# Optimization experiments

Measured on AMD Instinct MI355X. Metric: run time of the kernel, lower is better.

Reference implementation:

```python
import jax, jax.numpy as jnp
import numpy as np

B, T, E, S, D, HG = 16, 1024, 1024, 256, 512, 128
P_MIN, P_MAX, K_MAX, MAX_INNOV, EPS = 1e-6, 10.0, 1.0, 10.0, 1e-6


def setup_inputs() -> dict:
    key = jax.random.key(0)
    ks = jax.random.split(key, 16)
    g = lambda k, shape, fan: jax.random.normal(k, shape, jnp.float32) * np.float32(1.0 / np.sqrt(fan))
    # orthogonal init for the state-transition matrix A
    A = jnp.linalg.qr(jax.random.normal(ks[1], (S, S), jnp.float32))[0]
    return {
        "x": jax.random.normal(ks[0], (B, T, E), jnp.float32),
        "W_in": g(ks[2], (E, D), E), "b_in": jnp.zeros((D,), jnp.float32),
        "W_state": g(ks[3], (D, S), D), "b_state": jnp.zeros((S,), jnp.float32),
        "A": A, "H": g(ks[4], (D, S), D),
        "Q": jnp.full((S,), 0.1, jnp.float32), "R": jnp.full((D,), 0.1, jnp.float32),
        "W_z": g(ks[5], (HG, HG + S), HG + S), "W_r": g(ks[6], (HG, HG + S), HG + S),
        "W_h": g(ks[7], (HG, HG + S), HG + S),
        "b_z": jnp.zeros((HG,), jnp.float32), "b_r": jnp.zeros((HG,), jnp.float32),
        "b_h": jnp.zeros((HG,), jnp.float32),
        "W_out": g(ks[8], (HG, S), HG),
        "W_outp": g(ks[9], (D, E), D), "b_outp": jnp.zeros((E,), jnp.float32),
    }


def reference(x, W_in, b_in, W_state, b_state, A, H, Q, R,
              W_z, W_r, W_h, b_z, b_r, b_h, W_out, W_outp, b_outp):
    # input projection with GELU (Dense(d_inner, activation='gelu'))
    u = jax.nn.gelu(jnp.einsum("bte,ed->btd", x, W_in) + b_in)  # [B,T,D]
    q_sp = jax.nn.softplus(Q)                 # process noise, per state dim
    r_eff = jnp.mean(jax.nn.softplus(R))      # scalar effective measurement noise

    def step(carry, u_t):
        x_est, P, h = carry                   # [B,S], [B,S], [B,HG]
        # 1. state prediction (+ learned control input from measurement)
        x_pred = x_est @ A.T + u_t @ W_state + b_state          # [B,S]
        # 2. covariance prediction with clipping
        P_pred = jnp.clip(P + q_sp, P_MIN, P_MAX)                # [B,S]
        # 3. innovation (clipped for stability)
        y = jnp.clip(u_t - x_pred @ H.T, -MAX_INNOV, MAX_INNOV)  # [B,D]
        # 4. Kalman gain, bounded in [0, k_max]
        K = jnp.clip(P_pred / (P_pred + r_eff + EPS), 0.0, K_MAX)  # [B,S]
        # 5. state update: x_post = x_pred + K * (H^T @ innovation)
        x_post = x_pred + K * (y @ H)                            # [B,S]
        # 6. covariance update
        P_post = jnp.clip(P_pred * (1.0 - K), P_MIN, P_MAX)      # [B,S]
        # GRU gating over posterior state
        hx = jnp.concatenate([h, x_post], axis=-1)               # [B,HG+S]
        zg = jax.nn.sigmoid(hx @ W_z.T + b_z)
        rg = jax.nn.sigmoid(hx @ W_r.T + b_r)
        hc = jnp.tanh(jnp.concatenate([rg * h, x_post], axis=-1) @ W_h.T + b_h)
        h_new = (1.0 - zg) * h + zg * hc                         # [B,HG]
        # neural correction of state via GRU output projection
        x_final = x_post + h_new @ W_out                         # [B,S]
        return (x_final, P_post, h_new), x_final

    x0 = jnp.zeros((x.shape[0], S), x.dtype)
    P0 = jnp.ones((x.shape[0], S), x.dtype)   # identity covariance (diagonal)
    h0 = jnp.zeros((x.shape[0], HG), x.dtype)
    (_, _, _), xs = jax.lax.scan(step, (x0, P0, h0), jnp.swapaxes(u, 0, 1))
    xs = jnp.swapaxes(xs, 0, 1)               # [B,T,S]
    obs = jnp.einsum("bts,ds->btd", xs, H)    # reconstruct observation space
    out = jnp.einsum("btd,de->bte", obs, W_outp) + b_outp
    return out + x                            # residual connection
```

## Files before the change

kernel.cpp:

```cpp
#include <hip/hip_runtime.h>
#include <cstdint>
#include <cstddef>

#define NB 16
#define NT 1024
#define NE 1024
#define NS 256
#define ND 512
#define NH 128
#define T0 16

#define OFF_US   ((size_t)0)
#define OFF_HU   ((size_t)4194304)
#define OFF_U3   ((size_t)8388608)
#define OFF_KT   ((size_t)12582912)
#define OFF_HT   ((size_t)12845056)
#define OFF_AT   ((size_t)12976128)
#define OFF_G    ((size_t)13041664)
#define OFF_IG   ((size_t)13107200)
#define OFF_MINF ((size_t)13172736)
#define OFF_WZT  ((size_t)13238272)
#define OFF_WRT  ((size_t)13287424)
#define OFF_WHT  ((size_t)13336576)
#define OFF_HTWO ((size_t)13385728)
#define OFF_PACK ((size_t)13647872)

#define PK_A   0
#define PK_G   65536
#define PK_M   131072
#define PK_Z   196608
#define PK_R   245760
#define PK_H   294912
#define PK_O   344064
#define PK_WIN 376832
#define PK_WST 901120
#define PK_HM  1032192
#define PK_HTW 1163264


typedef short bf16x8 __attribute__((ext_vector_type(8)));
typedef float f32x4 __attribute__((ext_vector_type(4)));
typedef unsigned int u32x2 __attribute__((ext_vector_type(2)));

#define MFMA(a, b, c) __builtin_amdgcn_mfma_f32_16x16x32_bf16((a), (b), (c), 0, 0, 0)

#define SYNCW() do { \
    __builtin_amdgcn_sched_barrier(0); \
    asm volatile("s_waitcnt lgkmcnt(0)" ::: "memory"); \
    __builtin_amdgcn_s_barrier(); \
    __builtin_amdgcn_sched_barrier(0); \
} while (0)

__device__ __forceinline__ float gelu_tanh(float v) {
    const float c = 0.7978845608028654f;
    float t = tanhf(c * (v + 0.044715f * v * v * v));
    return 0.5f * v * (1.0f + t);
}
__device__ __forceinline__ float softplus_f(float x) {
    if (x > 20.0f) return x;
    return log1pf(expf(x));
}
__device__ __forceinline__ short f2bf_s(float f) {
    unsigned u = __float_as_uint(f);
    u += 0x7fffu + ((u >> 16) & 1u);
    return (short)(u >> 16);
}
__device__ __forceinline__ unsigned pk_bf(float a, float b) {
    return ((unsigned)(unsigned short)f2bf_s(b) << 16) | (unsigned)(unsigned short)f2bf_s(a);
}
__device__ __forceinline__ float exp2_hw(float x) {
    float r; asm("v_exp_f32 %0, %1" : "=v"(r) : "v"(x)); return r;
}
__device__ __forceinline__ float rcp_hw(float x) {
    float r; asm("v_rcp_f32 %0, %1" : "=v"(r) : "v"(x)); return r;
}
__device__ __forceinline__ f32x4 sig4(f32x4 x) {
    f32x4 o;
#pragma unroll
    for (int i = 0; i < 4; ++i)
        o[i] = rcp_hw(1.0f + exp2_hw(-1.442695040888963f * x[i]));
    return o;
}
__device__ __forceinline__ f32x4 tanh4(f32x4 x) {
    f32x4 o;
#pragma unroll
    for (int i = 0; i < 4; ++i) {
        float e = exp2_hw(2.885390081777927f * x[i]);
        o[i] = 1.0f - 2.0f * rcp_hw(e + 1.0f);
    }
    return o;
}
__device__ __forceinline__ void st_bf4(char* base, int stride, int row, int byteoff,
                                       const f32x4& v) {
    u32x2 p;
    p[0] = pk_bf(v[0], v[1]);
    p[1] = pk_bf(v[2], v[3]);
    *(u32x2*)(base + row * stride + byteoff) = p;
}

#define BFRAG(buf, STR, ks) (*(const bf16x8*)((buf) + (l & 15) * (STR) + (ks) * 64 + (l >> 4) * 16))
#define GFRAG(p, fi) (*(const bf16x8*)((p) + ((size_t)(fi) * 64 + l) * 8))
#define LFRAG(buf, fi) (*(const bf16x8*)((buf) + (size_t)(fi) * 1024 + l * 16))

__global__ __launch_bounds__(512) void k_precompute(const float* __restrict__ Q,
                                                    const float* __restrict__ R,
                                                    float* __restrict__ Kt) {
    __shared__ float red[512];
    __shared__ float r_eff_sh;
    const int t = threadIdx.x;
    red[t] = softplus_f(R[t]);
    __syncthreads();
    for (int s = 256; s > 0; s >>= 1) {
        if (t < s) red[t] += red[t + s];
        __syncthreads();
    }
    if (t == 0) r_eff_sh = red[0] / 512.0f;
    __syncthreads();
    const float r_eff = r_eff_sh;
    if (t < NS) {
        const float q = softplus_f(Q[t]);
        float P = 1.0f;
        for (int step = 0; step < NT; ++step) {
            float Pp = fminf(fmaxf(P + q, 1e-6f), 10.0f);
            float K  = fminf(fmaxf(Pp / (Pp + r_eff + 1e-6f), 0.0f), 1.0f);
            Kt[(size_t)step * NS + t] = K;
            P = fminf(fmaxf(Pp * (1.0f - K), 1e-6f), 10.0f);
        }
    }
}

__global__ void k_transpose(const float* __restrict__ in, float* __restrict__ outp,
                            int Rr, int Cc) {
    int i = blockIdx.x * 256 + threadIdx.x;
    if (i < Rr * Cc) {
        int r = i / Cc, c = i % Cc;
        outp[(size_t)c * Rr + r] = in[i];
    }
}

__global__ void k_ig(const float* __restrict__ G, const float* __restrict__ Kt,
                     float* __restrict__ IG) {
    int i = blockIdx.x * 256 + threadIdx.x;
    if (i >= NS * NS) return;
    int r = i >> 8, c = i & 255;
    float kinf = Kt[(size_t)(NT - 1) * NS + c];
    IG[i] = ((r == c) ? 1.0f : 0.0f) - G[i] * kinf;
}

__global__ void k_fuse(const float* __restrict__ us, const float* __restrict__ usG,
                       const float* __restrict__ Hu, const float* __restrict__ Kt,
                       float* __restrict__ u3) {
    int i = blockIdx.x * 256 + threadIdx.x;
    if (i >= NT * NB * NS) return;
    int s = i & 255;
    int tm = i >> 8;
    int m = tm & 15, t = tm >> 4;
    size_t src = ((size_t)m * NT + t) * NS + s;
    float k = Kt[(size_t)t * NS + s];
    u3[i] = us[src] + k * (Hu[src] - usG[src]);
}

__global__ void k_pack(const float* __restrict__ W, short* __restrict__ dst, int K, int N) {
    int f = blockIdx.x * 256 + threadIdx.x;
    if (f >= K * N) return;
    const int j = f & 7, l = (f >> 3) & 63, tile = f >> 9;
    const int KS = K >> 5;
    const int nt = tile / KS, ks = tile - nt * KS;
    const int k = ks * 32 + (l >> 4) * 8 + j;
    const int n = nt * 16 + (l & 15);
    dst[f] = f2bf_s(W[(size_t)k * N + n]);
}

__global__ __launch_bounds__(256) void k_mm(const float* __restrict__ Af,
                                            const short* __restrict__ Bpk,
                                            const float* __restrict__ bias,
                                            const float* __restrict__ resid,
                                            float* __restrict__ C,
                                            int N, int K, int act) {
    const int tid = threadIdx.x, w = tid >> 6, l = tid & 63;
    const int KS = K >> 5;
    const int mt = blockIdx.x * 4 + w;
    const int nt0 = blockIdx.y * 8;
    const float* arow = Af + (size_t)(mt * 16 + (l & 15)) * K + ((l >> 4) * 8);
    f32x4 acc[8];
#pragma unroll
    for (int j = 0; j < 8; ++j) acc[j] = (f32x4){0.f, 0.f, 0.f, 0.f};
    for (int ks = 0; ks < KS; ++ks) {
        const float* ap = arow + ks * 32;
        f32x4 a0 = *(const f32x4*)ap;
        f32x4 a1 = *(const f32x4*)(ap + 4);
        union { bf16x8 v; unsigned u[4]; } au;
        au.u[0] = pk_bf(a0[0], a0[1]); au.u[1] = pk_bf(a0[2], a0[3]);
        au.u[2] = pk_bf(a1[0], a1[1]); au.u[3] = pk_bf(a1[2], a1[3]);
#pragma unroll
        for (int j = 0; j < 8; ++j) {
            bf16x8 b = *(const bf16x8*)(Bpk + ((size_t)(nt0 + j) * KS + ks) * 512 + (size_t)l * 8);
            acc[j] = MFMA(b, au.v, acc[j]);
        }
    }
    const int m = mt * 16 + (l & 15);
    const int lg = l >> 4;
#pragma unroll
    for (int j = 0; j < 8; ++j) {
        const int n = (nt0 + j) * 16 + lg * 4;
        f32x4 v = acc[j];
        if (bias) v += *(const f32x4*)(bias + n);
        if (act) {
#pragma unroll
            for (int r = 0; r < 4; ++r) v[r] = gelu_tanh(v[r]);
        }
        if (resid) v += *(const f32x4*)(resid + (size_t)m * N + n);
        *(f32x4*)(C + (size_t)m * N + n) = v;
    }
}

__global__ __launch_bounds__(256) void k_gemm(const float* __restrict__ Am,
                                              const float* __restrict__ Bm,
                                              const float* __restrict__ bias,
                                              const float* __restrict__ resid,
                                              float* __restrict__ Cm,
                                              int M, int N, int K, int act) {
    __shared__ __align__(16) float As[16][68];
    __shared__ __align__(16) float Bs[16][68];
    const int tid = threadIdx.x;
    const int bn = blockIdx.x, bm = blockIdx.y;
    const int row0 = bm * 64, col0 = bn * 64;
    const int tx = tid & 15, ty = tid >> 4;
    const int ar = tid >> 2, ac = (tid & 3) << 2;
    const int bk = tid >> 4, bc = (tid & 15) << 2;

    float acc[4][4];
#pragma unroll
    for (int i = 0; i < 4; ++i)
#pragma unroll
        for (int j = 0; j < 4; ++j) acc[i][j] = 0.0f;

    for (int k0 = 0; k0 < K; k0 += 16) {
        float4 av = *(const float4*)(Am + (size_t)(row0 + ar) * K + k0 + ac);
        float4 bv = *(const float4*)(Bm + (size_t)(k0 + bk) * N + col0 + bc);
        As[ac + 0][ar] = av.x; As[ac + 1][ar] = av.y;
        As[ac + 2][ar] = av.z; As[ac + 3][ar] = av.w;
        *(float4*)&Bs[bk][bc] = bv;
        __syncthreads();
#pragma unroll
        for (int kk = 0; kk < 16; ++kk) {
            const float a0 = As[kk][ty * 4 + 0], a1 = As[kk][ty * 4 + 1];
            const float a2 = As[kk][ty * 4 + 2], a3 = As[kk][ty * 4 + 3];
            const float4 b4 = *(const float4*)&Bs[kk][tx * 4];
            acc[0][0] += a0 * b4.x; acc[0][1] += a0 * b4.y; acc[0][2] += a0 * b4.z; acc[0][3] += a0 * b4.w;
            acc[1][0] += a1 * b4.x; acc[1][1] += a1 * b4.y; acc[1][2] += a1 * b4.z; acc[1][3] += a1 * b4.w;
            acc[2][0] += a2 * b4.x; acc[2][1] += a2 * b4.y; acc[2][2] += a2 * b4.z; acc[2][3] += a2 * b4.w;
            acc[3][0] += a3 * b4.x; acc[3][1] += a3 * b4.y; acc[3][2] += a3 * b4.z; acc[3][3] += a3 * b4.w;
        }
        __syncthreads();
    }
#pragma unroll
    for (int i = 0; i < 4; ++i) {
        const int r = row0 + ty * 4 + i;
#pragma unroll
        for (int j = 0; j < 4; ++j) {
            const int c = col0 + tx * 4 + j;
            float v = acc[i][j];
            if (bias) v += bias[c];
            if (act) v = gelu_tanh(v);
            if (resid) v += resid[(size_t)r * N + c];
            Cm[(size_t)r * N + c] = v;
        }
    }
}

#define XE_STR 528
#define HB_STR 272

__global__ __launch_bounds__(512, 2) void k_scan_mfma(
    const short* __restrict__ pM, const short* __restrict__ pA, const short* __restrict__ pG,
    const short* __restrict__ pZ, const short* __restrict__ pR, const short* __restrict__ pH,
    const short* __restrict__ pO,
    const float* __restrict__ bz, const float* __restrict__ br, const float* __restrict__ bh,
    const float* __restrict__ us, const float* __restrict__ Hu, const float* __restrict__ u3,
    const float* __restrict__ Kt, float* __restrict__ xs)
{
    __shared__ __align__(16) char XE[16 * XE_STR];
    __shared__ __align__(16) char XT[16 * XE_STR];
    __shared__ __align__(16) char HBs[16 * HB_STR];
    __shared__ __align__(16) char RGs[16 * HB_STR];
    __shared__ __align__(16) char WHH[64 * 1024];

    const int tid = threadIdx.x, w = tid >> 6, l = tid & 63;
    const int m = l & 15, lg = l >> 4;
    const int c0 = 32 * w + 4 * lg;
    const int cg = 16 * w + 4 * lg;

    for (int i = tid; i < (16 * XE_STR) / 4; i += 512) ((int*)XE)[i] = 0;
    for (int i = tid; i < (16 * HB_STR) / 4; i += 512) ((int*)HBs)[i] = 0;
    for (int i = tid; i < 4096; i += 512) {
        int fi = i >> 6, ln = i & 63;
        int wv = fi >> 3, ks = fi & 7;
        ((int4*)WHH)[i] = *(const int4*)(pH + ((size_t)(wv * 12 + 4 + ks) * 64 + ln) * 8);
    }

    const f32x4 bzv = *(const f32x4*)(bz + cg);
    const f32x4 brv = *(const f32x4*)(br + cg);
    const f32x4 bhv = *(const f32x4*)(bh + cg);
    f32x4 hFr = {0.f, 0.f, 0.f, 0.f};
    __syncthreads();

    for (int t = 0; t < T0; ++t) {
        const float* usb = us + ((size_t)m * NT + t) * NS;
        const float* hub = Hu + ((size_t)m * NT + t) * NS;
        const float* ktb = Kt + (size_t)t * NS;
        f32x4 us0 = *(const f32x4*)(usb + c0), us1 = *(const f32x4*)(usb + c0 + 16);
        f32x4 hu0 = *(const f32x4*)(hub + c0), hu1 = *(const f32x4*)(hub + c0 + 16);
        f32x4 kv0 = *(const f32x4*)(ktb + c0), kv1 = *(const f32x4*)(ktb + c0 + 16);
        f32x4 p0 = {0.f,0.f,0.f,0.f}, p1 = {0.f,0.f,0.f,0.f};
#pragma unroll
        for (int ks = 0; ks < 8; ++ks) {
            bf16x8 xe = BFRAG(XE, XE_STR, ks);
            p0 = MFMA(GFRAG(pA, (2 * w + 0) * 8 + ks), xe, p0);
            p1 = MFMA(GFRAG(pA, (2 * w + 1) * 8 + ks), xe, p1);
        }
        p0 += us0; p1 += us1;
        st_bf4(XT, XE_STR, m, c0 * 2, p0);
        st_bf4(XT, XE_STR, m, (c0 + 16) * 2, p1);
        SYNCW();
        f32x4 g0 = {0.f,0.f,0.f,0.f}, g1 = {0.f,0.f,0.f,0.f};
#pragma unroll
        for (int ks = 0; ks < 8; ++ks) {
            bf16x8 xt = BFRAG(XT, XE_STR, ks);
            g0 = MFMA(GFRAG(pG, (2 * w + 0) * 8 + ks), xt, g0);
            g1 = MFMA(GFRAG(pG, (2 * w + 1) * 8 + ks), xt, g1);
        }
        f32x4 xq0 = p0 + kv0 * (hu0 - g0);
        f32x4 xq1 = p1 + kv1 * (hu1 - g1);
        st_bf4(XE, XE_STR, m, c0 * 2, xq0);
        st_bf4(XE, XE_STR, m, (c0 + 16) * 2, xq1);
        SYNCW();
        f32x4 za = bzv, ra = brv, hx = bhv;
#pragma unroll
        for (int ks = 0; ks < 4; ++ks) {
            bf16x8 hb = BFRAG(HBs, HB_STR, ks);
            za = MFMA(GFRAG(pZ, w * 12 + ks), hb, za);
            ra = MFMA(GFRAG(pR, w * 12 + ks), hb, ra);
        }
#pragma unroll
        for (int ks = 0; ks < 8; ++ks) {
            bf16x8 xef = BFRAG(XE, XE_STR, ks);
            za = MFMA(GFRAG(pZ, w * 12 + 4 + ks), xef, za);
            ra = MFMA(GFRAG(pR, w * 12 + 4 + ks), xef, ra);
            hx = MFMA(GFRAG(pH, w * 12 + 4 + ks), xef, hx);
        }
        f32x4 z = sig4(za), r = sig4(ra), rg = r * hFr;
        st_bf4(RGs, HB_STR, m, cg * 2, rg);
        SYNCW();
        f32x4 hc = hx;
#pragma unroll
        for (int ks = 0; ks < 4; ++ks)
            hc = MFMA(GFRAG(pH, w * 12 + ks), BFRAG(RGs, HB_STR, ks), hc);
        f32x4 hcv = tanh4(hc);
        f32x4 hn = hFr + z * (hcv - hFr);
        hFr = hn;
        st_bf4(HBs, HB_STR, m, cg * 2, hn);
        SYNCW();
#pragma unroll
        for (int ks = 0; ks < 4; ++ks) {
            bf16x8 hb2 = BFRAG(HBs, HB_STR, ks);
            xq0 = MFMA(GFRAG(pO, (2 * w + 0) * 4 + ks), hb2, xq0);
            xq1 = MFMA(GFRAG(pO, (2 * w + 1) * 4 + ks), hb2, xq1);
        }
        st_bf4(XE, XE_STR, m, c0 * 2, xq0);
        st_bf4(XE, XE_STR, m, (c0 + 16) * 2, xq1);
        {
            float* xb = xs + ((size_t)m * NT + t) * NS;
            *(f32x4*)(xb + c0) = xq0;
            *(f32x4*)(xb + c0 + 16) = xq1;
        }
        SYNCW();
    }

    bf16x8 rM0[8], rM1[8], rZx[8], rRx[8], rZh[4], rRh[4], rO0[4], rO1[4], rHh[4];
#pragma unroll
    for (int ks = 0; ks < 8; ++ks) {
        rM0[ks] = GFRAG(pM, (2 * w + 0) * 8 + ks);
        rM1[ks] = GFRAG(pM, (2 * w + 1) * 8 + ks);
        rZx[ks] = GFRAG(pZ, w * 12 + 4 + ks);
        rRx[ks] = GFRAG(pR, w * 12 + 4 + ks);
    }
#pragma unroll
    for (int ks = 0; ks < 4; ++ks) {
        rZh[ks] = GFRAG(pZ, w * 12 + ks);
        rRh[ks] = GFRAG(pR, w * 12 + ks);
        rO0[ks] = GFRAG(pO, (2 * w + 0) * 4 + ks);
        rO1[ks] = GFRAG(pO, (2 * w + 1) * 4 + ks);
        rHh[ks] = GFRAG(pH, w * 12 + ks);
    }

    f32x4 zh = bzv, rh = brv;
#pragma unroll
    for (int ks = 0; ks < 4; ++ks) {
        bf16x8 hb = BFRAG(HBs, HB_STR, ks);
        zh = MFMA(rZh[ks], hb, zh);
        rh = MFMA(rRh[ks], hb, rh);
    }

    f32x4 cu0 = *(const f32x4*)(u3 + (size_t)T0 * (NB * NS) + (size_t)m * NS + c0);
    f32x4 cu1 = *(const f32x4*)(u3 + (size_t)T0 * (NB * NS) + (size_t)m * NS + c0 + 16);

    for (int t = T0; t < NT; ++t) {
        const int tn = (t + 1 < NT) ? (t + 1) : t;
        const float* ubn = u3 + (size_t)tn * (NB * NS) + (size_t)m * NS;
        f32x4 nx0 = *(const f32x4*)(ubn + c0);
        f32x4 nx1 = *(const f32x4*)(ubn + c0 + 16);

        f32x4 xq0 = {0.f,0.f,0.f,0.f}, xq1 = {0.f,0.f,0.f,0.f};
#pragma unroll
        for (int ks = 0; ks < 8; ++ks) {
            bf16x8 xe = BFRAG(XE, XE_STR, ks);
            xq0 = MFMA(rM0[ks], xe, xq0);
            xq1 = MFMA(rM1[ks], xe, xq1);
        }
        xq0 += cu0; xq1 += cu1;
        st_bf4(XT, XE_STR, m, c0 * 2, xq0);
        st_bf4(XT, XE_STR, m, (c0 + 16) * 2, xq1);
        SYNCW();
        f32x4 za = zh, ra = rh, hx = bhv;
#pragma unroll
        for (int ks = 0; ks < 8; ++ks) {
            bf16x8 xt = BFRAG(XT, XE_STR, ks);
            za = MFMA(rZx[ks], xt, za);
            ra = MFMA(rRx[ks], xt, ra);
            hx = MFMA(LFRAG(WHH, w * 8 + ks), xt, hx);
        }
        f32x4 z = sig4(za), r = sig4(ra), rg = r * hFr;
        st_bf4(RGs, HB_STR, m, cg * 2, rg);
        SYNCW();
        f32x4 hc = hx;
#pragma unroll
        for (int ks = 0; ks < 4; ++ks)
            hc = MFMA(rHh[ks], BFRAG(RGs, HB_STR, ks), hc);
        f32x4 hcv = tanh4(hc);
        f32x4 hn = hFr + z * (hcv - hFr);
        hFr = hn;
        st_bf4(HBs, HB_STR, m, cg * 2, hn);
        SYNCW();
        f32x4 zhN = bzv, rhN = brv;
#pragma unroll
        for (int ks = 0; ks < 4; ++ks) {
            bf16x8 hb2 = BFRAG(HBs, HB_STR, ks);
            xq0 = MFMA(rO0[ks], hb2, xq0);
            xq1 = MFMA(rO1[ks], hb2, xq1);
            zhN = MFMA(rZh[ks], hb2, zhN);
            rhN = MFMA(rRh[ks], hb2, rhN);
        }
        st_bf4(XE, XE_STR, m, c0 * 2, xq0);
        st_bf4(XE, XE_STR, m, (c0 + 16) * 2, xq1);
        {
            float* xb = xs + ((size_t)m * NT + t) * NS;
            *(f32x4*)(xb + c0) = xq0;
            *(f32x4*)(xb + c0 + 16) = xq1;
        }
        zh = zhN; rh = rhN;
        cu0 = nx0; cu1 = nx1;
        SYNCW();
    }
}

extern "C" void kernel_launch(void* const* d_in, const int* in_sizes, int n_in,
                              void* d_out, int out_size, void* d_ws, size_t ws_size,
                              hipStream_t stream) {
    (void)in_sizes; (void)n_in; (void)out_size; (void)ws_size;
    const float* x       = (const float*)d_in[0];
    const float* W_in    = (const float*)d_in[1];
    const float* b_in    = (const float*)d_in[2];
    const float* W_state = (const float*)d_in[3];
    const float* b_state = (const float*)d_in[4];
    const float* A       = (const float*)d_in[5];
    const float* H       = (const float*)d_in[6];
    const float* Q       = (const float*)d_in[7];
    const float* R       = (const float*)d_in[8];
    const float* W_z     = (const float*)d_in[9];
    const float* W_r     = (const float*)d_in[10];
    const float* W_h     = (const float*)d_in[11];
    const float* b_z     = (const float*)d_in[12];
    const float* b_r     = (const float*)d_in[13];
    const float* b_h     = (const float*)d_in[14];
    const float* W_out   = (const float*)d_in[15];
    const float* W_outp  = (const float*)d_in[16];
    const float* b_outp  = (const float*)d_in[17];
    float* out = (float*)d_out;
    float* w = (float*)d_ws;

    float* us   = w + OFF_US;
    float* Hu   = w + OFF_HU;
    float* u3   = w + OFF_U3;
    float* Kt   = w + OFF_KT;
    float* Ht   = w + OFF_HT;
    float* At   = w + OFF_AT;
    float* G    = w + OFF_G;
    float* IG   = w + OFF_IG;
    float* Minf = w + OFF_MINF;
    float* Wzt  = w + OFF_WZT;
    float* Wrt  = w + OFF_WRT;
    float* Wht  = w + OFF_WHT;
    float* HtWo = w + OFF_HTWO;
    short* pk   = (short*)(w + OFF_PACK);

    float* xs  = w + OFF_US;
    float* usG = out + (size_t)4194304;
    float* u   = out + (size_t)8388608;

    const int M = NB * NT;

    hipLaunchKernelGGL(k_precompute, dim3(1), dim3(512), 0, stream, Q, R, Kt);
    hipLaunchKernelGGL(k_transpose, dim3((NS * NS + 255) / 256), dim3(256), 0, stream, A, At, NS, NS);
    hipLaunchKernelGGL(k_transpose, dim3((ND * NS + 255) / 256), dim3(256), 0, stream, H, Ht, ND, NS);
    hipLaunchKernelGGL(k_transpose, dim3((NH * 384 + 255) / 256), dim3(256), 0, stream, W_z, Wzt, NH, 384);
    hipLaunchKernelGGL(k_transpose, dim3((NH * 384 + 255) / 256), dim3(256), 0, stream, W_r, Wrt, NH, 384);
    hipLaunchKernelGGL(k_transpose, dim3((NH * 384 + 255) / 256), dim3(256), 0, stream, W_h, Wht, NH, 384);
    hipLaunchKernelGGL(k_gemm, dim3(NS / 64, NS / 64), dim3(256), 0, stream,
                       Ht, H, nullptr, nullptr, G, NS, NS, ND, 0);
    hipLaunchKernelGGL(k_gemm, dim3(NE / 64, NS / 64), dim3(256), 0, stream,
                       Ht, W_outp, nullptr, nullptr, HtWo, NS, NE, ND, 0);
    hipLaunchKernelGGL(k_ig, dim3(256), dim3(256), 0, stream, G, Kt, IG);
    hipLaunchKernelGGL(k_gemm, dim3(NS / 64, NS / 64), dim3(256), 0, stream,
                       At, IG, nullptr, nullptr, Minf, NS, NS, NS, 0);
    hipLaunchKernelGGL(k_pack, dim3((NS * NS + 255) / 256), dim3(256), 0, stream, At, pk + PK_A, NS, NS);
    hipLaunchKernelGGL(k_pack, dim3((NS * NS + 255) / 256), dim3(256), 0, stream, G, pk + PK_G, NS, NS);
    hipLaunchKernelGGL(k_pack, dim3((NS * NS + 255) / 256), dim3(256), 0, stream, Minf, pk + PK_M, NS, NS);
    hipLaunchKernelGGL(k_pack, dim3((384 * NH + 255) / 256), dim3(256), 0, stream, Wzt, pk + PK_Z, 384, NH);
    hipLaunchKernelGGL(k_pack, dim3((384 * NH + 255) / 256), dim3(256), 0, stream, Wrt, pk + PK_R, 384, NH);
    hipLaunchKernelGGL(k_pack, dim3((384 * NH + 255) / 256), dim3(256), 0, stream, Wht, pk + PK_H, 384, NH);
    hipLaunchKernelGGL(k_pack, dim3((NH * NS + 255) / 256), dim3(256), 0, stream, W_out, pk + PK_O, NH, NS);
    hipLaunchKernelGGL(k_pack, dim3((NE * ND + 255) / 256), dim3(256), 0, stream, W_in, pk + PK_WIN, NE, ND);
    hipLaunchKernelGGL(k_pack, dim3((ND * NS + 255) / 256), dim3(256), 0, stream, W_state, pk + PK_WST, ND, NS);
    hipLaunchKernelGGL(k_pack, dim3((ND * NS + 255) / 256), dim3(256), 0, stream, H, pk + PK_HM, ND, NS);
    hipLaunchKernelGGL(k_pack, dim3((NS * NE + 255) / 256), dim3(256), 0, stream, HtWo, pk + PK_HTW, NS, NE);
    hipLaunchKernelGGL(k_mm, dim3(M / 64, ND / 128), dim3(256), 0, stream,
                       x, pk + PK_WIN, b_in, nullptr, u, ND, NE, 1);
    hipLaunchKernelGGL(k_mm, dim3(M / 64, NS / 128), dim3(256), 0, stream,
                       u, pk + PK_WST, b_state, nullptr, us, NS, ND, 0);
    hipLaunchKernelGGL(k_mm, dim3(M / 64, NS / 128), dim3(256), 0, stream,
                       u, pk + PK_HM, nullptr, nullptr, Hu, NS, ND, 0);
    hipLaunchKernelGGL(k_mm, dim3(M / 64, NS / 128), dim3(256), 0, stream,
                       us, pk + PK_G, nullptr, nullptr, usG, NS, NS, 0);
    hipLaunchKernelGGL(k_fuse, dim3((NT * NB * NS) / 256), dim3(256), 0, stream,
                       us, usG, Hu, Kt, u3);
    hipLaunchKernelGGL(k_scan_mfma, dim3(1), dim3(512), 0, stream,
                       pk + PK_M, pk + PK_A, pk + PK_G, pk + PK_Z, pk + PK_R, pk + PK_H,
                       pk + PK_O,
                       b_z, b_r, b_h, us, Hu, u3, Kt, xs);
    hipLaunchKernelGGL(k_mm, dim3(M / 64, NE / 128), dim3(256), 0, stream,
                       xs, pk + PK_HTW, b_outp, x, out, NE, NS, 0);
}
```

Baseline: 3.778 ms.

## Fold steady-state transition into GRU gate weights to shorten scan critical path

The GRU gate inputs from x_post are rewritten algebraically as Minf·x_prev + u3. The gate weights are premultiplied by the steady-state matrix (Mg = Minf·Wg), and the u3-dependent gate contributions plus biases are precomputed for all timesteps in a parallel GEMM (ug). The scan loop can then compute state and gate preactivations from the previous state in one MFMA pass, removing one LDS round-trip and barrier per step on the serial critical path. The cost is more MFMA work per step, an extra LDS-resident weight block, and a precomputed gate tensor streamed from global memory. Products are reassociated in bf16, which may shift numerics.

```diff
diff --git a/kernel.cpp b/kernel.cpp
--- a/kernel.cpp
+++ b/kernel.cpp
@@ -23,7 +23,10 @@
 #define OFF_WRT  ((size_t)13287424)
 #define OFF_WHT  ((size_t)13336576)
 #define OFF_HTWO ((size_t)13385728)
-#define OFF_PACK ((size_t)13647872)
+#define OFF_WG   ((size_t)13647872)
+#define OFF_BG   ((size_t)13746176)
+#define OFF_MG   ((size_t)13746688)
+#define OFF_PACK ((size_t)13844992)
 
 #define PK_A   0
 #define PK_G   65536
@@ -36,6 +39,8 @@
 #define PK_WST 901120
 #define PK_HM  1032192
 #define PK_HTW 1163264
+#define PK_MG  1425408
+#define PK_WG  1523712
 
 
 typedef short bf16x8 __attribute__((ext_vector_type(8)));
@@ -158,6 +163,23 @@
     size_t src = ((size_t)m * NT + t) * NS + s;
     float k = Kt[(size_t)t * NS + s];
     u3[i] = us[src] + k * (Hu[src] - usG[src]);
+}
+
+__global__ void k_build(const float* __restrict__ Wzt, const float* __restrict__ Wrt,
+                        const float* __restrict__ Wht,
+                        const float* __restrict__ bz, const float* __restrict__ br,
+                        const float* __restrict__ bh,
+                        float* __restrict__ Wg, float* __restrict__ bg) {
+    int i = blockIdx.x * 256 + threadIdx.x;
+    if (i < 256 * 384) {
+        int s = i / 384, j = i % 384;
+        const float* src = (j < 128) ? Wzt : (j < 256) ? Wrt : Wht;
+        int jj = j & 127;
+        Wg[i] = src[(size_t)(128 + s) * 128 + jj];
+    }
+    if (i < 384) {
+        bg[i] = (i < 128) ? bz[i] : (i < 256) ? br[i - 128] : bh[i - 256];
+    }
 }
 
 __global__ void k_pack(const float* __restrict__ W, short* __restrict__ dst, int K, int N) {
@@ -275,16 +297,18 @@
 __global__ __launch_bounds__(512, 2) void k_scan_mfma(
     const short* __restrict__ pM, const short* __restrict__ pA, const short* __restrict__ pG,
     const short* __restrict__ pZ, const short* __restrict__ pR, const short* __restrict__ pH,
-    const short* __restrict__ pO,
+    const short* __restrict__ pO, const short* __restrict__ pMG,
     const float* __restrict__ bz, const float* __restrict__ br, const float* __restrict__ bh,
-    const float* __restrict__ us, const float* __restrict__ Hu, const float* __restrict__ u3,
+    const float* __restrict__ us, const float* __restrict__ Hu,
+    const float* __restrict__ u3, const float* __restrict__ ug,
     const float* __restrict__ Kt, float* __restrict__ xs)
 {
     __shared__ __align__(16) char XE[16 * XE_STR];
     __shared__ __align__(16) char XT[16 * XE_STR];
     __shared__ __align__(16) char HBs[16 * HB_STR];
     __shared__ __align__(16) char RGs[16 * HB_STR];
-    __shared__ __align__(16) char WHH[64 * 1024];
+    __shared__ __align__(16) char MHH[64 * 1024];
+    __shared__ __align__(16) char WH2[32 * 1024];
 
     const int tid = threadIdx.x, w = tid >> 6, l = tid & 63;
     const int m = l & 15, lg = l >> 4;
@@ -296,7 +320,12 @@
     for (int i = tid; i < 4096; i += 512) {
         int fi = i >> 6, ln = i & 63;
         int wv = fi >> 3, ks = fi & 7;
-        ((int4*)WHH)[i] = *(const int4*)(pH + ((size_t)(wv * 12 + 4 + ks) * 64 + ln) * 8);
+        ((int4*)MHH)[i] = *(const int4*)(pMG + ((size_t)((16 + wv) * 8 + ks) * 64 + ln) * 8);
+    }
+    for (int i = tid; i < 2048; i += 512) {
+        int fi = i >> 6, ln = i & 63;
+        int nt = fi >> 2, ks = fi & 3;
+        ((int4*)WH2)[i] = *(const int4*)(pH + ((size_t)(nt * 12 + ks) * 64 + ln) * 8);
     }
 
     const f32x4 bzv = *(const f32x4*)(bz + cg);
@@ -377,13 +406,13 @@
         SYNCW();
     }
 
-    bf16x8 rM0[8], rM1[8], rZx[8], rRx[8], rZh[4], rRh[4], rO0[4], rO1[4], rHh[4];
+    bf16x8 rM0[8], rM1[8], rMZ[8], rMR[8], rZh[4], rRh[4], rO0[4], rO1[4];
 #pragma unroll
     for (int ks = 0; ks < 8; ++ks) {
         rM0[ks] = GFRAG(pM, (2 * w + 0) * 8 + ks);
         rM1[ks] = GFRAG(pM, (2 * w + 1) * 8 + ks);
-        rZx[ks] = GFRAG(pZ, w * 12 + 4 + ks);
-        rRx[ks] = GFRAG(pR, w * 12 + 4 + ks);
+        rMZ[ks] = GFRAG(pMG, w * 8 + ks);
+        rMR[ks] = GFRAG(pMG, (8 + w) * 8 + ks);
     }
 #pragma unroll
     for (int ks = 0; ks < 4; ++ks) {
@@ -391,10 +420,9 @@
         rRh[ks] = GFRAG(pR, w * 12 + ks);
         rO0[ks] = GFRAG(pO, (2 * w + 0) * 4 + ks);
         rO1[ks] = GFRAG(pO, (2 * w + 1) * 4 + ks);
-        rHh[ks] = GFRAG(pH, w * 12 + ks);
-    }
-
-    f32x4 zh = bzv, rh = brv;
+    }
+
+    f32x4 zh = {0.f,0.f,0.f,0.f}, rh = {0.f,0.f,0.f,0.f};
 #pragma unroll
     for (int ks = 0; ks < 4; ++ks) {
         bf16x8 hb = BFRAG(HBs, HB_STR, ks);
@@ -402,47 +430,41 @@
         rh = MFMA(rRh[ks], hb, rh);
     }
 
-    f32x4 cu0 = *(const f32x4*)(u3 + (size_t)T0 * (NB * NS) + (size_t)m * NS + c0);
-    f32x4 cu1 = *(const f32x4*)(u3 + (size_t)T0 * (NB * NS) + (size_t)m * NS + c0 + 16);
-
     for (int t = T0; t < NT; ++t) {
-        const int tn = (t + 1 < NT) ? (t + 1) : t;
-        const float* ubn = u3 + (size_t)tn * (NB * NS) + (size_t)m * NS;
-        f32x4 nx0 = *(const f32x4*)(ubn + c0);
-        f32x4 nx1 = *(const f32x4*)(ubn + c0 + 16);
+        const float* ubase = u3 + ((size_t)(t * NB) + m) * NS;
+        const float* gbase = ug + ((size_t)(t * NB) + m) * 384;
+        f32x4 cu0 = *(const f32x4*)(ubase + c0);
+        f32x4 cu1 = *(const f32x4*)(ubase + c0 + 16);
+        f32x4 cz  = *(const f32x4*)(gbase + cg);
+        f32x4 cr  = *(const f32x4*)(gbase + 128 + cg);
+        f32x4 chx = *(const f32x4*)(gbase + 256 + cg);
 
         f32x4 xq0 = {0.f,0.f,0.f,0.f}, xq1 = {0.f,0.f,0.f,0.f};
+        f32x4 za = zh, ra = rh, hx = {0.f,0.f,0.f,0.f};
 #pragma unroll
         for (int ks = 0; ks < 8; ++ks) {
             bf16x8 xe = BFRAG(XE, XE_STR, ks);
+            bf16x8 mh = LFRAG(MHH, w * 8 + ks);
             xq0 = MFMA(rM0[ks], xe, xq0);
             xq1 = MFMA(rM1[ks], xe, xq1);
-        }
-        xq0 += cu0; xq1 += cu1;
-        st_bf4(XT, XE_STR, m, c0 * 2, xq0);
-        st_bf4(XT, XE_STR, m, (c0 + 16) * 2, xq1);
-        SYNCW();
-        f32x4 za = zh, ra = rh, hx = bhv;
-#pragma unroll
-        for (int ks = 0; ks < 8; ++ks) {
-            bf16x8 xt = BFRAG(XT, XE_STR, ks);
-            za = MFMA(rZx[ks], xt, za);
-            ra = MFMA(rRx[ks], xt, ra);
-            hx = MFMA(LFRAG(WHH, w * 8 + ks), xt, hx);
-        }
+            za  = MFMA(rMZ[ks], xe, za);
+            ra  = MFMA(rMR[ks], xe, ra);
+            hx  = MFMA(mh,      xe, hx);
+        }
+        xq0 += cu0; xq1 += cu1; za += cz; ra += cr;
         f32x4 z = sig4(za), r = sig4(ra), rg = r * hFr;
         st_bf4(RGs, HB_STR, m, cg * 2, rg);
         SYNCW();
-        f32x4 hc = hx;
+        f32x4 hc = hx + chx;
 #pragma unroll
         for (int ks = 0; ks < 4; ++ks)
-            hc = MFMA(rHh[ks], BFRAG(RGs, HB_STR, ks), hc);
+            hc = MFMA(LFRAG(WH2, w * 4 + ks), BFRAG(RGs, HB_STR, ks), hc);
         f32x4 hcv = tanh4(hc);
         f32x4 hn = hFr + z * (hcv - hFr);
         hFr = hn;
         st_bf4(HBs, HB_STR, m, cg * 2, hn);
         SYNCW();
-        f32x4 zhN = bzv, rhN = brv;
+        f32x4 zhN = {0.f,0.f,0.f,0.f}, rhN = {0.f,0.f,0.f,0.f};
 #pragma unroll
         for (int ks = 0; ks < 4; ++ks) {
             bf16x8 hb2 = BFRAG(HBs, HB_STR, ks);
@@ -459,7 +481,6 @@
             *(f32x4*)(xb + c0 + 16) = xq1;
         }
         zh = zhN; rh = rhN;
-        cu0 = nx0; cu1 = nx1;
         SYNCW();
     }
 }
@@ -502,9 +523,13 @@
     float* Wrt  = w + OFF_WRT;
     float* Wht  = w + OFF_WHT;
     float* HtWo = w + OFF_HTWO;
+    float* Wg   = w + OFF_WG;
+    float* bg   = w + OFF_BG;
+    float* Mg   = w + OFF_MG;
     short* pk   = (short*)(w + OFF_PACK);
 
     float* xs  = w + OFF_US;
+    float* ug  = out;
     float* usG = out + (size_t)4194304;
     float* u   = out + (size_t)8388608;
 
@@ -523,6 +548,10 @@
     hipLaunchKernelGGL(k_ig, dim3(256), dim3(256), 0, stream, G, Kt, IG);
     hipLaunchKernelGGL(k_gemm, dim3(NS / 64, NS / 64), dim3(256), 0, stream,
                        At, IG, nullptr, nullptr, Minf, NS, NS, NS, 0);
+    hipLaunchKernelGGL(k_build, dim3(384), dim3(256), 0, stream,
+                       Wzt, Wrt, Wht, b_z, b_r, b_h, Wg, bg);
+    hipLaunchKernelGGL(k_gemm, dim3(384 / 64, NS / 64), dim3(256), 0, stream,
+                       Minf, Wg, nullptr, nullptr, Mg, NS, 384, NS, 0);
     hipLaunchKernelGGL(k_pack, dim3((NS * NS + 255) / 256), dim3(256), 0, stream, At, pk + PK_A, NS, NS);
     hipLaunchKernelGGL(k_pack, dim3((NS * NS + 255) / 256), dim3(256), 0, stream, G, pk + PK_G, NS, NS);
     hipLaunchKernelGGL(k_pack, dim3((NS * NS + 255) / 256), dim3(256), 0, stream, Minf, pk + PK_M, NS, NS);
@@ -534,6 +563,8 @@
     hipLaunchKernelGGL(k_pack, dim3((ND * NS + 255) / 256), dim3(256), 0, stream, W_state, pk + PK_WST, ND, NS);
     hipLaunchKernelGGL(k_pack, dim3((ND * NS + 255) / 256), dim3(256), 0, stream, H, pk + PK_HM, ND, NS);
     hipLaunchKernelGGL(k_pack, dim3((NS * NE + 255) / 256), dim3(256), 0, stream, HtWo, pk + PK_HTW, NS, NE);
+    hipLaunchKernelGGL(k_pack, dim3((NS * 384 + 255) / 256), dim3(256), 0, stream, Mg, pk + PK_MG, NS, 384);
+    hipLaunchKernelGGL(k_pack, dim3((NS * 384 + 255) / 256), dim3(256), 0, stream, Wg, pk + PK_WG, NS, 384);
     hipLaunchKernelGGL(k_mm, dim3(M / 64, ND / 128), dim3(256), 0, stream,
                        x, pk + PK_WIN, b_in, nullptr, u, ND, NE, 1);
     hipLaunchKernelGGL(k_mm, dim3(M / 64, NS / 128), dim3(256), 0, stream,
@@ -544,10 +575,12 @@
                        us, pk + PK_G, nullptr, nullptr, usG, NS, NS, 0);
     hipLaunchKernelGGL(k_fuse, dim3((NT * NB * NS) / 256), dim3(256), 0, stream,
                        us, usG, Hu, Kt, u3);
+    hipLaunchKernelGGL(k_mm, dim3(M / 64, 384 / 128), dim3(256), 0, stream,
+                       u3, pk + PK_WG, bg, nullptr, ug, 384, NS, 0);
     hipLaunchKernelGGL(k_scan_mfma, dim3(1), dim3(512), 0, stream,
                        pk + PK_M, pk + PK_A, pk + PK_G, pk + PK_Z, pk + PK_R, pk + PK_H,
-                       pk + PK_O,
-                       b_z, b_r, b_h, us, Hu, u3, Kt, xs);
+                       pk + PK_O, pk + PK_MG,
+                       b_z, b_r, b_h, us, Hu, u3, ug, Kt, xs);
     hipLaunchKernelGGL(k_mm, dim3(M / 64, NE / 128), dim3(256), 0, stream,
                        xs, pk + PK_HTW, b_outp, x, out, NE, NS, 0);
 }
```

Result: slower. 5.154 ms (+36.4%).
